# Kernel optimization log

Measured on AMD Instinct MI355X. Metric: run time of the kernel, lower is better.

## Reference

```python
import jax, jax.numpy as jnp
import numpy as np

B, D, C_IN = 2, 64, 4
N1, N2, N3, N4 = 32, 64, 96, 128
MQ, K = 1024, 5
DN = ('NCDHW', 'OIDHW', 'NCDHW')
PAD = [(2, 2)] * 3  # centered 5^3 kernel, matches Minkowski offsets in [-2, 2]


def setup_inputs() -> dict:
    rng = np.random.default_rng(0)
    mask = rng.random((B, D, D, D)) < 0.2
    x_feat = (rng.standard_normal((B, C_IN, D, D, D)) * mask[:, None]).astype(np.float32)
    Q_F = rng.random((B, MQ, 2)).astype(np.float32)  # per-point quality features (2 channels)

    def conv(cin, cout):
        w = (rng.standard_normal((cout, cin, K, K, K)) / np.sqrt(cin * K ** 3)).astype(np.float32)
        b = (0.01 * rng.standard_normal(cout)).astype(np.float32)
        return w, b

    def gdn(c):
        beta = np.ones(c, np.float32)
        gamma = (1e-4 * rng.random((c, c, K, K, K))).astype(np.float32)
        gamma[np.arange(c), np.arange(c), K // 2, K // 2, K // 2] += 0.1
        return beta, gamma

    w1, b1 = conv(C_IN, N1)
    w2, b2 = conv(N1, N2)
    w3, b3 = conv(N2, N3)
    w4, b4 = conv(N3, N4)
    beta1, gamma1 = gdn(N1)
    beta2, gamma2 = gdn(N2)
    beta3, gamma3 = gdn(N3)
    out = dict(x_feat=x_feat, mask=mask, Q_F=Q_F,
               w1=w1, b1=b1, w2=w2, b2=b2, w3=w3, b3=b3, w4=w4, b4=b4,
               beta1=beta1, gamma1=gamma1, beta2=beta2, gamma2=gamma2,
               beta3=beta3, gamma3=gamma3)
    return {k: jnp.asarray(v) for k, v in out.items()}


def _conv3d(x, w, b, stride):
    y = jax.lax.conv_general_dilated(x, w, (stride,) * 3, PAD, dimension_numbers=DN)
    return y + b[None, :, None, None, None]


def _pool_mask(m):
    # Minkowski stride-2 output coords = any occupied input in each 2x2x2 cell
    b, d = m.shape[0], m.shape[1]
    return m.reshape(b, d // 2, 2, d // 2, 2, d // 2, 2).max(axis=(2, 4, 6))


def _gdn(x, beta, gamma, scale, m):
    # conditional GDN: y = x / sqrt(beta + conv5(gamma, x^2)), scaled per batch by q[:,0]
    den = jax.lax.conv_general_dilated(x * x, gamma, (1, 1, 1), PAD, dimension_numbers=DN)
    y = x * jax.lax.rsqrt(beta[None, :, None, None, None] + den)
    return y * scale * m[:, None]


def reference(x_feat, mask, Q_F, w1, b1, w2, b2, w3, b3, w4, b4,
              beta1, gamma1, beta2, gamma2, beta3, gamma3):
    m0 = mask.astype(x_feat.dtype)
    q = jnp.mean(Q_F, axis=1)[None]                       # [1, B, 2]: per-batch mean of Q.F
    scale = q[0, :, 0][:, None, None, None, None]         # per-batch conditional scale

    c0 = m0.sum(axis=(1, 2, 3))                           # count_per_batch(x)
    m1 = _pool_mask(m0)
    x = _gdn(_conv3d(x_feat, w1, b1, 2) * m1[:, None], beta1, gamma1, scale, m1)
    c1 = m1.sum(axis=(1, 2, 3))
    m2 = _pool_mask(m1)
    x = _gdn(_conv3d(x, w2, b2, 2) * m2[:, None], beta2, gamma2, scale, m2)
    c2 = m2.sum(axis=(1, 2, 3))
    m3 = _pool_mask(m2)
    x = _gdn(_conv3d(x, w3, b3, 2) * m3[:, None], beta3, gamma3, scale, m3)
    x = _conv3d(x, w4, b4, 1) * m3[:, None]               # stride-1 conv keeps coords
    k = jnp.stack([c2, c1, c0]).astype(jnp.int32)         # k.reverse() in the original
    return x, q, k
```

## Files before the change

### kernel.cpp

```cpp
#include <hip/hip_runtime.h>
#include <math.h>

constexpr int Bn  = 2;
constexpr int CIN = 4;
constexpr int MQn = 1024;
constexpr int D0 = 64, D1 = 32, D2 = 16, D3 = 8;

constexpr int OUT_X = 0;
constexpr int OUT_Q = 131072;
constexpr int OUT_K = 131076;

constexpr size_t OFF_CNT   = 0;
constexpr size_t OFF_ZERO  = 8;
constexpr size_t OFF_D1    = 16;
constexpr size_t OFF_T2    = OFF_D1 + 2097152;
constexpr size_t OFF_D2    = OFF_T2 + 524288;
constexpr size_t OFF_T3    = OFF_D2 + 524288;
constexpr size_t OFF_D3    = OFF_T3 + 98304;
constexpr size_t ZERO_END  = OFF_D3 + 98304;
constexpr size_t OFF_SCALE = 3342360;
constexpr size_t OFF_M1    = 3342368;
constexpr size_t OFF_M2    = OFF_M1 + 65536;
constexpr size_t OFF_M3    = OFF_M2 + 8192;
constexpr size_t OFF_T1    = OFF_M3 + 1024;
constexpr size_t OFF_Y1    = OFF_T1 + 2097152;
constexpr size_t OFF_Y2    = OFF_Y1 + 2097152;
constexpr size_t OFF_SQ1   = OFF_Y2 + 524288;
constexpr size_t OFF_SQ2   = OFF_SQ1 + 1048576;
constexpr size_t OFF_SQ3   = OFF_SQ2 + 262144;
constexpr size_t OFF_Y3C   = OFF_SQ3 + 49152;
constexpr size_t OFF_W1T   = OFF_Y3C + 49152;
constexpr size_t OFF_W2T   = OFF_W1T + 16000;
constexpr size_t OFF_W3T   = OFF_W2T + 256000;
constexpr size_t OFF_WB1   = OFF_W3T + 768000;
constexpr size_t OFF_WB2   = OFF_WB1 + 64000;
constexpr size_t OFF_WB3   = OFF_WB2 + 256000;
constexpr size_t OFF_WB4   = OFF_WB3 + 576000;
constexpr size_t OFF_P2    = 12248736;
constexpr size_t OFF_Y1HL  = OFF_P2 + 3145728;
constexpr size_t OFF_WB2S  = OFF_Y1HL + 3145728;

typedef float v4f __attribute__((ext_vector_type(4)));
typedef __attribute__((ext_vector_type(8)))  short bf16x8v;
typedef __attribute__((ext_vector_type(16))) float f32x16v;

__device__ __forceinline__ void async_copy4(const float* g, float* l) {
    __builtin_amdgcn_global_load_lds(
        (const __attribute__((address_space(1))) void*)g,
        (__attribute__((address_space(3))) void*)l, 4, 0, 0);
}
__device__ __forceinline__ void async_copy16(const float* g, float* l) {
    __builtin_amdgcn_global_load_lds(
        (const __attribute__((address_space(1))) void*)g,
        (__attribute__((address_space(3))) void*)l, 16, 0, 0);
}
__device__ __forceinline__ unsigned short f2bf(float f) {
    unsigned u = __float_as_uint(f);
    return (unsigned short)((u + 0x7FFFu + ((u >> 16) & 1u)) >> 16);
}
__device__ __forceinline__ float bf2f(unsigned short h) {
    return __uint_as_float((unsigned)h << 16);
}

__global__ void qmean_kernel(const float* __restrict__ QF, float* __restrict__ out_q,
                             float* __restrict__ scale) {
    int b = blockIdx.x >> 1, c = blockIdx.x & 1;
    float s = 0.f;
    for (int m = threadIdx.x; m < MQn; m += blockDim.x)
        s += QF[(b * MQn + m) * 2 + c];
    __shared__ float sh[256];
    sh[threadIdx.x] = s;
    __syncthreads();
    for (int st = 128; st > 0; st >>= 1) {
        if (threadIdx.x < st) sh[threadIdx.x] += sh[threadIdx.x + st];
        __syncthreads();
    }
    if (threadIdx.x == 0) {
        float mean = sh[0] / (float)MQn;
        out_q[b * 2 + c] = mean;
        if (c == 0) scale[b] = mean;
    }
}

__global__ void mask_pool1_kernel(const float* __restrict__ xf, float* __restrict__ m1,
                                  float* __restrict__ c0) {
    int idx = blockIdx.x * blockDim.x + threadIdx.x;
    int b = idx >> 15;
    int v = idx & 32767;
    int oz = v >> 10, oy = (v >> 5) & 31, ox = v & 31;
    float cnt = 0.f, mx = 0.f;
    for (int dz = 0; dz < 2; ++dz)
        for (int dy = 0; dy < 2; ++dy)
            for (int dx = 0; dx < 2; ++dx) {
                int z = 2 * oz + dz, y = 2 * oy + dy, x = 2 * ox + dx;
                size_t base = (size_t)b * CIN * D0 * D0 * D0 + ((size_t)z * D0 + y) * D0 + x;
                bool occ = false;
                for (int c = 0; c < CIN; ++c)
                    occ = occ || (xf[base + (size_t)c * D0 * D0 * D0] != 0.f);
                if (occ) { cnt += 1.f; mx = 1.f; }
            }
    m1[idx] = mx;
    __shared__ float sh[256];
    sh[threadIdx.x] = cnt;
    __syncthreads();
    for (int st = 128; st > 0; st >>= 1) {
        if (threadIdx.x < st) sh[threadIdx.x] += sh[threadIdx.x + st];
        __syncthreads();
    }
    if (threadIdx.x == 0) atomicAdd(&c0[b], sh[0]);
}

__global__ void pool_kernel(const float* __restrict__ min_, float* __restrict__ mout,
                            float* __restrict__ cacc, int Din) {
    int Do = Din >> 1;
    int per = Do * Do * Do;
    int idx = blockIdx.x * blockDim.x + threadIdx.x;
    int b = idx / per;
    int v = idx % per;
    int oz = v / (Do * Do), oy = (v / Do) % Do, ox = v % Do;
    float s = 0.f, mx = 0.f;
    for (int dz = 0; dz < 2; ++dz)
        for (int dy = 0; dy < 2; ++dy)
            for (int dx = 0; dx < 2; ++dx) {
                float val = min_[(((size_t)b * Din + 2 * oz + dz) * Din + 2 * oy + dy) * Din + 2 * ox + dx];
                s += val;
                mx = fmaxf(mx, val);
            }
    mout[idx] = mx;
    __shared__ float sh[256];
    sh[threadIdx.x] = s;
    __syncthreads();
    for (int st = 128; st > 0; st >>= 1) {
        if (threadIdx.x < st) sh[threadIdx.x] += sh[threadIdx.x + st];
        __syncthreads();
    }
    if (threadIdx.x == 0) atomicAdd(&cacc[b], sh[0]);
}

__global__ void writek_kernel(const float* __restrict__ cnt, float* __restrict__ outk) {
    int i = threadIdx.x;
    if (i < 6) {
        int row = i >> 1, b = i & 1;
        float v = (row == 0) ? cnt[4 + b] : (row == 1 ? cnt[2 + b] : cnt[b]);
        outk[i] = v;
    }
}

constexpr int FS1 = 0,       FE1 = 16000;
constexpr int FS2 = 16000,   FE2 = 272000;
constexpr int FS3 = 272000,  FE3 = 1040000;
__global__ __launch_bounds__(256) void wtrans_all_kernel(
        const float* __restrict__ w1, const float* __restrict__ w2,
        const float* __restrict__ w3, float* __restrict__ ws) {
    int idx = blockIdx.x * 256 + threadIdx.x;
    if (idx >= FE3) return;
    const float* src; float* dst; int cin, local;
    if (idx < FE1)      { src = w1; dst = ws + OFF_W1T; cin = 4;  local = idx - FS1; }
    else if (idx < FE2) { src = w2; dst = ws + OFF_W2T; cin = 32; local = idx - FS2; }
    else                { src = w3; dst = ws + OFF_W3T; cin = 64; local = idx - FS3; }
    int per = cin * 125;
    int co = local / per;
    int r  = local % per;
    int ci = r / 125, tap = r % 125;
    int chunk = co >> 4, j = co & 15;
    dst[(((size_t)chunk * cin + ci) * 125 + tap) * 16 + j] = src[local];
}

constexpr int MS1 = 0,        ME1 = 128000;
constexpr int MS2 = 128000,   ME2 = 640000;
constexpr int MS3 = 640000,   ME3 = 1792000;
constexpr int MS4 = 1792000,  ME4 = 3328000;
__global__ __launch_bounds__(256) void mwtrans_all_kernel(
        const float* __restrict__ g1, const float* __restrict__ g2,
        const float* __restrict__ g3, const float* __restrict__ w4,
        float* __restrict__ ws) {
    int idx = blockIdx.x * 256 + threadIdx.x;
    if (idx >= ME4) return;
    const float* src; unsigned short* dst; int nchn, cin, o;
    if (idx < ME1)      { src = g1; dst = (unsigned short*)(ws + OFF_WB1); nchn = 1; cin = 32; o = idx - MS1; }
    else if (idx < ME2) { src = g2; dst = (unsigned short*)(ws + OFF_WB2); nchn = 2; cin = 64; o = idx - MS2; }
    else if (idx < ME3) { src = g3; dst = (unsigned short*)(ws + OFF_WB3); nchn = 3; cin = 96; o = idx - MS3; }
    else                { src = w4; dst = (unsigned short*)(ws + OFF_WB4); nchn = 4; cin = 96; o = idx - MS4; }
    int j  = o & 7;
    int kc = (o >> 3) & 1;
    int n  = (o >> 4) & 31;
    int q  = o >> 9;
    int tap = q % 125;
    int q2  = q / 125;
    int nch = q2 % nchn;
    int cs  = q2 / nchn;
    int co = nch * 32 + n;
    int ci = cs * 16 + kc * 8 + j;
    dst[o] = f2bf(src[((size_t)co * cin + ci) * 125 + tap]);
}

constexpr int W2S_N = 768000;
__global__ __launch_bounds__(256) void w2s_kernel(const float* __restrict__ w2,
        unsigned short* __restrict__ dst) {
    int o = blockIdx.x * 256 + threadIdx.x;
    if (o >= W2S_N) return;
    int j = o & 7; int kc = (o >> 3) & 1; int n = (o >> 4) & 31; int q = o >> 9;
    int tap = q % 125; int q2 = q / 125; int c = q2 & 1; int cs = q2 >> 1;
    int co = c * 32 + n;
    int e = cs * 16 + kc * 8 + j;
    int ci = e & 31;
    float wv = w2[((size_t)co * 32 + ci) * 125 + tap];
    unsigned short h = f2bf(wv);
    if (e >= 64) h = f2bf(wv - bf2f(h));
    dst[o] = h;
}

template<int CINt, int COUTt, int DIN, int DOUT, int STRIDE, int CIG, bool SQW>
__global__ __launch_bounds__(256, 4) void conv_tile_kernel(
    const float* __restrict__ in, const float* __restrict__ wt,
    const float* __restrict__ bb, const float* __restrict__ mask,
    const float* __restrict__ zerow, float* __restrict__ out,
    unsigned short* __restrict__ sqcl)
{
    constexpr int TZO = 4, TY = 8, TX = 8;
    constexpr int LZ = (STRIDE == 1) ? TZO + 4 : 2 * TZO + 3;
    constexpr int LY = (STRIDE == 1) ? TY + 4 : 2 * TY + 3;
    constexpr int LX = (STRIDE == 1) ? TX + 4 : 2 * TX + 3;
    constexpr int LXP = (STRIDE == 2) ? (LX + 1) / 2 : 0;
    constexpr int ROWLEN = (STRIDE == 2) ? 2 * LXP : LX;
    constexpr int LN = LZ * LY * ROWLEN;
    constexpr int NLOAD = (LN + 255) / 256;
    constexpr int PADN = NLOAD * 256;
    constexpr int NTZ = DOUT / TZO, NTY = DOUT / TY, NTX = DOUT / TX;
    constexpr int NT = NTZ * NTY * NTX;
    constexpr int NCHk = COUTt / 16;
    constexpr int CIPER = CINt / CIG;
    __shared__ float sh[2][PADN];
    __shared__ float wbuf[2][2048];

    int tile  = blockIdx.x % NT;
    int chunk = (blockIdx.x / NT) % NCHk;
    int cig   = (blockIdx.x / (NT * NCHk)) % CIG;
    int b     = blockIdx.x / (NT * NCHk * CIG);
    int tz0 = (tile / (NTY * NTX)) * TZO;
    int ty0 = ((tile / NTX) % NTY) * TY;
    int tx0 = (tile % NTX) * TX;
    int co0 = chunk * 16;

    int tid = threadIdx.x;
    int tx = tid & (TX - 1);
    int ty = (tid >> 3) & (TY - 1);
    int tz = tid >> 6;

    int iz0 = tz0 * STRIDE - 2, iy0 = ty0 * STRIDE - 2, ix0 = tx0 * STRIDE - 2;

    int goff[NLOAD];
#pragma unroll
    for (int k = 0; k < NLOAD; ++k) {
        int i = tid + k * 256;
        int c = i % ROWLEN; int rem = i / ROWLEN;
        int ly = rem % LY, lz = rem / LY;
        int lx;
        if (STRIDE == 2) { int p = c / LXP, xp = c % LXP; lx = 2 * xp + p; }
        else lx = c;
        int gz = iz0 + lz, gy = iy0 + ly, gx = ix0 + lx;
        bool valid = (i < LN) && (lx < LX) &&
                     (unsigned)gz < (unsigned)DIN && (unsigned)gy < (unsigned)DIN &&
                     (unsigned)gx < (unsigned)DIN;
        goff[k] = valid ? ((gz * DIN + gy) * DIN + gx) : -1;
    }

    int ci0 = cig * CIPER;
    auto stage = [&](int ci, int buf) {
        const float* base = in + (size_t)(b * CINt + ci) * DIN * DIN * DIN;
        float* dst = &sh[buf][0];
#pragma unroll
        for (int k = 0; k < NLOAD; ++k) {
            const float* g = (goff[k] >= 0) ? (base + goff[k]) : zerow;
            async_copy4(g, &dst[k * 256 + tid]);
        }
        const float* wsrc = wt + (size_t)(chunk * CINt + ci) * 2000;
#pragma unroll
        for (int k = 0; k < 2; ++k) {
            int f0 = (k * 256 + tid) * 4;
            const float* g = (f0 < 2000) ? (wsrc + f0) : zerow;
            async_copy16(g, &wbuf[buf][f0]);
        }
    };

    float acc[16];
#pragma unroll
    for (int j = 0; j < 16; ++j) acc[j] = 0.f;

    stage(ci0, 0);
#pragma unroll 1
    for (int i = 0; i < CIPER; ++i) {
        int cur = i & 1;
        __syncthreads();
        if (i + 1 < CIPER) stage(ci0 + i + 1, cur ^ 1);
        const float* shc = &sh[cur][0];
        const float* wb = &wbuf[cur][0];
#pragma unroll 1
        for (int kz = 0; kz < 5; ++kz) {
#pragma unroll 1
            for (int ky = 0; ky < 5; ++ky) {
                const float* rp = shc + ((tz * STRIDE + kz) * LY + ty * STRIDE + ky) * ROWLEN + tx;
                const float* wrow = wb + (kz * 5 + ky) * 5 * 16;
#pragma unroll
                for (int kx = 0; kx < 5; ++kx) {
                    float d = (STRIDE == 2) ? rp[(kx & 1) * LXP + (kx >> 1)] : rp[kx];
#pragma unroll
                    for (int q = 0; q < 4; ++q) {
                        v4f w = *(const v4f*)&wrow[kx * 16 + q * 4];
                        acc[4 * q + 0] = fmaf(d, w.x, acc[4 * q + 0]);
                        acc[4 * q + 1] = fmaf(d, w.y, acc[4 * q + 1]);
                        acc[4 * q + 2] = fmaf(d, w.z, acc[4 * q + 2]);
                        acc[4 * q + 3] = fmaf(d, w.w, acc[4 * q + 3]);
                    }
                }
            }
        }
    }

    int z = tz0 + tz, y = ty0 + ty, x = tx0 + tx;
    size_t sp = ((size_t)z * DOUT + y) * DOUT + x;
    if (CIG > 1) {
#pragma unroll
        for (int j = 0; j < 16; ++j) {
            size_t oidx = (size_t)(b * COUTt + co0 + j) * DOUT * DOUT * DOUT + sp;
            atomicAdd(&out[oidx], acc[j]);
        }
    } else {
        float mval = mask[(size_t)b * DOUT * DOUT * DOUT + sp];
        float vals[16];
#pragma unroll
        for (int j = 0; j < 16; ++j) {
            int co = co0 + j;
            size_t oidx = (size_t)(b * COUTt + co) * DOUT * DOUT * DOUT + sp;
            vals[j] = (acc[j] + bb[co]) * mval;
            out[oidx] = vals[j];
        }
        if (SQW) {
            bf16x8v s0, s1;
#pragma unroll
            for (int j = 0; j < 8; ++j) {
                s0[j] = (short)f2bf(vals[j] * vals[j]);
                s1[j] = (short)f2bf(vals[j + 8] * vals[j + 8]);
            }
            size_t cl = ((size_t)b * DOUT * DOUT * DOUT + sp) * COUTt + co0;
            *(bf16x8v*)(sqcl + cl) = s0;
            *(bf16x8v*)(sqcl + cl + 8) = s1;
        }
    }
}

__global__ __launch_bounds__(128) void gdn_cl1_kernel(const float* __restrict__ t,
        const float* __restrict__ den, const float* __restrict__ beta,
        const float* __restrict__ scale, unsigned short* __restrict__ yhl) {
    int idx = blockIdx.x * 128 + threadIdx.x;
    int sp = idx & 32767; int b = idx >> 15;
    float sc = scale[b];
    bf16x8v blk[12];
#pragma unroll
    for (int g = 0; g < 4; ++g) {
#pragma unroll
        for (int j = 0; j < 8; ++j) {
            int ci = g * 8 + j;
            size_t p = (size_t)(b * 32 + ci) * 32768 + sp;
            float v = t[p] * rsqrtf(beta[ci] + den[p]) * sc;
            unsigned short h = f2bf(v);
            blk[g][j] = (short)h;
            blk[4 + g][j] = (short)f2bf(v - bf2f(h));
            blk[8 + g][j] = (short)h;
        }
    }
    unsigned short* o = yhl + (size_t)idx * 96;
#pragma unroll
    for (int g = 0; g < 12; ++g) *(bf16x8v*)(o + g * 8) = blk[g];
}

template<int CINe, int COUTt, int DIN, int DOUT>
__global__ __launch_bounds__(256) void mconv_s2_kernel(
    const unsigned short* __restrict__ in,
    const unsigned short* __restrict__ wb,
    const float* __restrict__ zerow,
    float* __restrict__ pout)
{
    constexpr int NCH = COUTt / 32;
    constexpr int NTZ = DOUT / 4, NTY = DOUT / 4, NTX = DOUT / 8;
    constexpr int NT = NTZ * NTY * NTX * Bn;
    constexpr int VOX = DOUT * DOUT * DOUT;

    int tile = blockIdx.x % NT; int cs = blockIdx.x / NT;
    int r = tile;
    int tx0 = (r % NTX) * 8; r /= NTX;
    int ty0 = (r % NTY) * 4; r /= NTY;
    int tz0 = (r % NTZ) * 4; int b = r / NTZ;

    int tid = threadIdx.x;
    int lane = tid & 63, w = tid >> 6;
    int n = lane & 31, kc = lane >> 5;
    int oz = tz0 + w, oy = ty0 + (n >> 3), ox = tx0 + (n & 7);

    f32x16v acc[NCH];
#pragma unroll
    for (int c = 0; c < NCH; ++c)
#pragma unroll
        for (int i = 0; i < 16; ++i) acc[c][i] = 0.f;

#pragma unroll 1
    for (int kz = 0; kz < 5; ++kz) {
        int gz = 2 * oz + kz - 2;
        bool zok = (unsigned)gz < (unsigned)DIN;
#pragma unroll 1
        for (int ky = 0; ky < 5; ++ky) {
            int gy = 2 * oy + ky - 2;
            bool zyok = zok && ((unsigned)gy < (unsigned)DIN);
            long long rowbase = (((long long)(b * DIN + gz) * DIN + gy) * DIN) * CINe
                                + cs * 16 + kc * 8;
#pragma unroll
            for (int kx = 0; kx < 5; ++kx) {
                int gx = 2 * ox + kx - 2;
                bool ok = zyok && ((unsigned)gx < (unsigned)DIN);
                const unsigned short* g = ok ? in + (rowbase + (long long)gx * CINe)
                                             : (const unsigned short*)zerow;
                bf16x8v dfrag = *(const bf16x8v*)g;
                int tap = (kz * 5 + ky) * 5 + kx;
#pragma unroll
                for (int c = 0; c < NCH; ++c) {
                    const unsigned short* wp =
                        wb + (((size_t)(cs * NCH + c) * 125 + tap) << 9) + n * 16 + kc * 8;
                    bf16x8v wfrag = *(const bf16x8v*)wp;
                    acc[c] = __builtin_amdgcn_mfma_f32_32x32x16_bf16(wfrag, dfrag, acc[c], 0, 0, 0);
                }
            }
        }
    }

    int sp = (oz * DOUT + oy) * DOUT + ox;
#pragma unroll
    for (int c = 0; c < NCH; ++c) {
#pragma unroll
        for (int rr = 0; rr < 16; ++rr) {
            int co = c * 32 + (rr & 3) + 8 * (rr >> 2) + 4 * kc;
            pout[((size_t)(cs * Bn + b) * COUTt + co) * VOX + sp] = acc[c][rr];
        }
    }
}

__global__ __launch_bounds__(256) void red_epi2_kernel(const float* __restrict__ P,
        const float* __restrict__ bias, const float* __restrict__ mask,
        float* __restrict__ buf, unsigned short* __restrict__ sqcl) {
    constexpr int VOX = 4096;
    constexpr int NTOT = Bn * 64 * VOX;
    int idx = blockIdx.x * 256 + threadIdx.x;
    if (idx >= NTOT) return;
    int sp = idx % VOX;
    int co = (idx / VOX) & 63;
    int b = idx / (VOX * 64);
    float s = 0.f;
#pragma unroll
    for (int k = 0; k < 6; ++k) s += P[(size_t)k * NTOT + idx];
    float v = (s + bias[co]) * mask[b * VOX + sp];
    buf[idx] = v;
    sqcl[((size_t)b * VOX + sp) * 64 + co] = f2bf(v * v);
}

template<int CINt, int COUTt, int Dd, int TZ, int YB, int CIG, int ZSPL>
__global__ __launch_bounds__(256) void mconv_kernel(
    const unsigned short* __restrict__ in,
    const unsigned short* __restrict__ wb,
    const float* __restrict__ zerow,
    float* __restrict__ dout)
{
    constexpr int NCH = COUTt / 32;
    constexpr int LZ = TZ + 4, LYH = YB * 4 + 4, LXH = 12;
    constexpr int HV = LZ * LYH * LXH;
    constexpr int UN = 2 * HV;
    constexpr int NLOAD = (UN + 255) / 256;
    constexpr int NTZ = Dd / TZ, NTY = Dd / (YB * 4), NTX = Dd / 8;
    constexpr int NT = NTZ * NTY * NTX * Bn;
    __shared__ unsigned short lds[NLOAD * 256 * 8];

    int bid = blockIdx.x;
    int tile = bid % NT; int rest = bid / NT;
    int cs = rest % CIG; int zig = rest / CIG;
    int r = tile;
    int tx0 = (r % NTX) * 8; r /= NTX;
    int ty0 = (r % NTY) * (YB * 4); r /= NTY;
    int tz0 = (r % NTZ) * TZ; int b = r / NTZ;

    int tid = threadIdx.x;
    int iz0 = tz0 - 2, iy0 = ty0 - 2, ix0 = tx0 - 2;
#pragma unroll
    for (int k = 0; k < NLOAD; ++k) {
        int u = tid + k * 256;
        int v = u >> 1, half = u & 1;
        int lx = v % LXH; int t = v / LXH;
        int ly = t % LYH, lz = t / LYH;
        int gz = iz0 + lz, gy = iy0 + ly, gx = ix0 + lx;
        bool valid = (v < HV) &&
                     (unsigned)gz < (unsigned)Dd && (unsigned)gy < (unsigned)Dd &&
                     (unsigned)gx < (unsigned)Dd;
        const unsigned short* g = valid
            ? in + ((((size_t)b * Dd + gz) * Dd + gy) * Dd + gx) * CINt + cs * 16 + half * 8
            : (const unsigned short*)zerow;
        async_copy16((const float*)g, (float*)&lds[(size_t)u * 8]);
    }
    __syncthreads();

    int lane = tid & 63, w = tid >> 6;
    int zz = (YB == 1) ? w : (w >> 1);
    int yb = (YB == 1) ? 0 : (w & 1);
    int n = lane & 31, kc = lane >> 5;
    int vy = yb * 4 + (n >> 3), vx = n & 7;

    f32x16v acc[NCH];
#pragma unroll
    for (int c = 0; c < NCH; ++c)
#pragma unroll
        for (int i = 0; i < 16; ++i) acc[c][i] = 0.f;

    int kzlo = (ZSPL == 5) ? zig : 0;
    int kzhi = (ZSPL == 5) ? zig + 1 : 5;
#pragma unroll 1
    for (int kz = kzlo; kz < kzhi; ++kz) {
#pragma unroll 1
        for (int ky = 0; ky < 5; ++ky) {
            int hvrow = ((zz + kz) * LYH + (vy + ky)) * LXH + vx;
#pragma unroll
            for (int kx = 0; kx < 5; ++kx) {
                bf16x8v dfrag = *(const bf16x8v*)&lds[(size_t)(hvrow + kx) * 16 + kc * 8];
                int tap = (kz * 5 + ky) * 5 + kx;
#pragma unroll
                for (int c = 0; c < NCH; ++c) {
                    const unsigned short* wp =
                        wb + (((size_t)(cs * NCH + c) * 125 + tap) << 9) + n * 16 + kc * 8;
                    bf16x8v wfrag = *(const bf16x8v*)wp;
                    acc[c] = __builtin_amdgcn_mfma_f32_32x32x16_bf16(wfrag, dfrag, acc[c], 0, 0, 0);
                }
            }
        }
    }

    int sp = ((tz0 + zz) * Dd + (ty0 + vy)) * Dd + (tx0 + vx);
#pragma unroll
    for (int c = 0; c < NCH; ++c) {
#pragma unroll
        for (int rr = 0; rr < 16; ++rr) {
            int co = c * 32 + (rr & 3) + 8 * (rr >> 2) + 4 * kc;
            atomicAdd(&dout[(size_t)(b * COUTt + co) * Dd * Dd * Dd + sp], acc[c][rr]);
        }
    }
}

template<int COUTt, int DOUT, bool SQ>
__global__ __launch_bounds__(256) void conv_epi_kernel(float* __restrict__ buf,
        const float* __restrict__ bias, const float* __restrict__ mask,
        unsigned short* __restrict__ sqcl) {
    constexpr int VOX = DOUT * DOUT * DOUT;
    int idx = blockIdx.x * 256 + threadIdx.x;
    if (idx >= Bn * COUTt * VOX) return;
    int sp = idx % VOX;
    int co = (idx / VOX) % COUTt;
    int b = idx / (VOX * COUTt);
    float v = (buf[idx] + bias[co]) * mask[b * VOX + sp];
    buf[idx] = v;
    if (SQ) sqcl[((size_t)b * VOX + sp) * COUTt + co] = f2bf(v * v);
}

template<int COUTt, int DOUT, bool CL>
__global__ __launch_bounds__(256) void gdn_epi_kernel(const float* __restrict__ t,
        const float* __restrict__ den, const float* __restrict__ beta,
        const float* __restrict__ scale, float* __restrict__ y,
        unsigned short* __restrict__ ycl) {
    constexpr int VOX = DOUT * DOUT * DOUT;
    int idx = blockIdx.x * 256 + threadIdx.x;
    if (idx >= Bn * COUTt * VOX) return;
    int sp = idx % VOX;
    int co = (idx / VOX) % COUTt;
    int b = idx / (VOX * COUTt);
    float v = t[idx] * rsqrtf(beta[co] + den[idx]) * scale[b];
    if (CL) ycl[((size_t)b * VOX + sp) * COUTt + co] = f2bf(v);
    else    y[idx] = v;
}

extern "C" void kernel_launch(void* const* d_in, const int* in_sizes, int n_in,
                              void* d_out, int out_size, void* d_ws, size_t ws_size,
                              hipStream_t stream) {
    const float* x_feat = (const float*)d_in[0];
    const float* QF     = (const float*)d_in[2];
    const float* w1 = (const float*)d_in[3];  const float* b1 = (const float*)d_in[4];
    const float* w2 = (const float*)d_in[5];  const float* b2 = (const float*)d_in[6];
    const float* w3 = (const float*)d_in[7];  const float* b3 = (const float*)d_in[8];
    const float* w4 = (const float*)d_in[9];  const float* b4 = (const float*)d_in[10];
    const float* beta1 = (const float*)d_in[11]; const float* gamma1 = (const float*)d_in[12];
    const float* beta2 = (const float*)d_in[13]; const float* gamma2 = (const float*)d_in[14];
    const float* beta3 = (const float*)d_in[15]; const float* gamma3 = (const float*)d_in[16];

    float* out = (float*)d_out;
    float* ws = (float*)d_ws;
    float* cnt   = ws + OFF_CNT;
    float* zerow = ws + OFF_ZERO;
    float* scale = ws + OFF_SCALE;
    float* m1 = ws + OFF_M1;  float* m2 = ws + OFF_M2;  float* m3 = ws + OFF_M3;
    float* t1 = ws + OFF_T1;  float* d1 = ws + OFF_D1;
    float* t2 = ws + OFF_T2;  float* d2 = ws + OFF_D2;  float* y2 = ws + OFF_Y2;
    float* t3 = ws + OFF_T3;  float* d3 = ws + OFF_D3;
    float* p2 = ws + OFF_P2;
    unsigned short* sq1 = (unsigned short*)(ws + OFF_SQ1);
    unsigned short* sq2 = (unsigned short*)(ws + OFF_SQ2);
    unsigned short* sq3 = (unsigned short*)(ws + OFF_SQ3);
    unsigned short* y3c = (unsigned short*)(ws + OFF_Y3C);
    unsigned short* y1hl = (unsigned short*)(ws + OFF_Y1HL);
    float* w1T = ws + OFF_W1T; float* w3T = ws + OFF_W3T;
    unsigned short* wb1 = (unsigned short*)(ws + OFF_WB1);
    unsigned short* wb2 = (unsigned short*)(ws + OFF_WB2);
    unsigned short* wb3 = (unsigned short*)(ws + OFF_WB3);
    unsigned short* wb4 = (unsigned short*)(ws + OFF_WB4);
    unsigned short* wb2s = (unsigned short*)(ws + OFF_WB2S);

    hipMemsetAsync(ws, 0, ZERO_END * sizeof(float), stream);
    hipMemsetAsync(out + OUT_X, 0, 131072 * sizeof(float), stream);

    qmean_kernel<<<4, 256, 0, stream>>>(QF, out + OUT_Q, scale);
    mask_pool1_kernel<<<256, 256, 0, stream>>>(x_feat, m1, cnt + 0);
    pool_kernel<<<32, 256, 0, stream>>>(m1, m2, cnt + 2, D1);
    pool_kernel<<<4, 256, 0, stream>>>(m2, m3, cnt + 4, D2);
    writek_kernel<<<1, 64, 0, stream>>>(cnt, out + OUT_K);

    wtrans_all_kernel<<<(FE3 + 255) / 256, 256, 0, stream>>>(w1, w2, w3, ws);
    mwtrans_all_kernel<<<(ME4 + 255) / 256, 256, 0, stream>>>(gamma1, gamma2, gamma3, w4, ws);
    w2s_kernel<<<(W2S_N + 255) / 256, 256, 0, stream>>>(w2, wb2s);

    conv_tile_kernel<4, 32, 64, 32, 2, 1, true>
        <<<512, 256, 0, stream>>>(x_feat, w1T, b1, m1, zerow, t1, sq1);
    mconv_kernel<32, 32, 32, 4, 1, 2, 1>
        <<<1024, 256, 0, stream>>>(sq1, wb1, zerow, d1);
    gdn_cl1_kernel<<<512, 128, 0, stream>>>(t1, d1, beta1, scale, y1hl);

    mconv_s2_kernel<96, 64, 32, 16>
        <<<64 * 6, 256, 0, stream>>>(y1hl, wb2s, zerow, p2);
    red_epi2_kernel<<<2048, 256, 0, stream>>>(p2, b2, m2, t2, sq2);
    mconv_kernel<64, 64, 16, 4, 1, 4, 1>
        <<<256, 256, 0, stream>>>(sq2, wb2, zerow, d2);
    gdn_epi_kernel<64, 16, false><<<2048, 256, 0, stream>>>(t2, d2, beta2, scale, y2, nullptr);

    conv_tile_kernel<64, 96, 16, 8, 2, 8, false>
        <<<192, 256, 0, stream>>>(y2, w3T, nullptr, nullptr, zerow, t3, nullptr);
    conv_epi_kernel<96, 8, true><<<384, 256, 0, stream>>>(t3, b3, m3, sq3);
    mconv_kernel<96, 96, 8, 2, 2, 6, 5>
        <<<240, 256, 0, stream>>>(sq3, wb3, zerow, d3);
    gdn_epi_kernel<96, 8, true><<<384, 256, 0, stream>>>(t3, d3, beta3, scale, nullptr, y3c);

    mconv_kernel<96, 128, 8, 2, 2, 6, 5>
        <<<240, 256, 0, stream>>>(y3c, wb4, zerow, out + OUT_X);
    conv_epi_kernel<128, 8, false><<<512, 256, 0, stream>>>(out + OUT_X, b4, m3, nullptr);
}
```

Measured before the change: 472.2 us.

## Move first stride-2 conv to bf16 MFMA with split hi/lo channels-last input

Replaces the fp32 tiled first convolution with an MFMA kernel. The input is first converted to channels-last bf16 hi/lo pairs packed into 8 K-lanes, and the weights get a matching hi/lo layout, so each tap is a single 32x32x16 MFMA. The epilogue applies bias and mask and writes both t1 and the bf16 squared features. This adds two preprocessing kernels and reads global memory directly without LDS reuse, and the bf16 split trades a little precision (the lo*lo term is dropped) for matrix-core throughput.

```diff
diff --git a/kernel.cpp b/kernel.cpp
--- a/kernel.cpp
+++ b/kernel.cpp
@@ -39,9 +39,11 @@
 constexpr size_t OFF_P2    = 12248736;
 constexpr size_t OFF_Y1HL  = OFF_P2 + 3145728;
 constexpr size_t OFF_WB2S  = OFF_Y1HL + 3145728;
+constexpr size_t OFF_WB1S  = OFF_WB2S + 384000;
 
 typedef float v4f __attribute__((ext_vector_type(4)));
 typedef __attribute__((ext_vector_type(8)))  short bf16x8v;
+typedef __attribute__((ext_vector_type(4)))  short bf16x4v;
 typedef __attribute__((ext_vector_type(16))) float f32x16v;
 
 __device__ __forceinline__ void async_copy4(const float* g, float* l) {
@@ -210,6 +212,101 @@
     dst[o] = h;
 }
 
+constexpr int W1S_N = 64000;
+__global__ __launch_bounds__(256) void w1s_kernel(const float* __restrict__ w1,
+        unsigned short* __restrict__ dst) {
+    int o = blockIdx.x * 256 + threadIdx.x;
+    if (o >= W1S_N) return;
+    int j = o & 7; int kc = (o >> 3) & 1; int n = (o >> 4) & 31; int tap = o >> 9;
+    int ci = j & 3;
+    unsigned short h;
+    float wv = w1[((size_t)n * 4 + ci) * 125 + tap];
+    unsigned short hi = f2bf(wv);
+    if (kc == 0)       h = hi;
+    else if (j < 4)    h = f2bf(wv - bf2f(hi));
+    else               h = 0;
+    dst[o] = h;
+}
+
+__global__ __launch_bounds__(256) void xcl_kernel(const float* __restrict__ xf,
+        unsigned short* __restrict__ xcl) {
+    int idx = blockIdx.x * 256 + threadIdx.x;
+    int s = idx & 262143; int b = idx >> 18;
+    bf16x8v o;
+#pragma unroll
+    for (int ci = 0; ci < 4; ++ci) {
+        float f = xf[((size_t)(b * 4 + ci) << 18) + s];
+        unsigned short h = f2bf(f);
+        o[ci] = (short)h;
+        o[4 + ci] = (short)f2bf(f - bf2f(h));
+    }
+    *(bf16x8v*)(xcl + (size_t)idx * 8) = o;
+}
+
+__global__ __launch_bounds__(256) void mconv1_s2_kernel(
+    const unsigned short* __restrict__ xcl,
+    const unsigned short* __restrict__ wb,
+    const float* __restrict__ bias, const float* __restrict__ mask,
+    const float* __restrict__ zerow,
+    float* __restrict__ t1, unsigned short* __restrict__ sqcl)
+{
+    constexpr int DIN = 64, DOUT = 32;
+    constexpr int NTX = 4, NTY = 8;
+    int r = blockIdx.x;
+    int tx0 = (r % NTX) * 8; r /= NTX;
+    int ty0 = (r % NTY) * 4; r /= NTY;
+    int tz0 = (r % 8) * 4;   int b = r / 8;
+
+    int tid = threadIdx.x;
+    int lane = tid & 63, w = tid >> 6;
+    int n = lane & 31, kc = lane >> 5;
+    int oz = tz0 + w, oy = ty0 + (n >> 3), ox = tx0 + (n & 7);
+
+    f32x16v acc;
+#pragma unroll
+    for (int i = 0; i < 16; ++i) acc[i] = 0.f;
+
+#pragma unroll 1
+    for (int kz = 0; kz < 5; ++kz) {
+        int gz = 2 * oz + kz - 2;
+        bool zok = (unsigned)gz < (unsigned)DIN;
+#pragma unroll 1
+        for (int ky = 0; ky < 5; ++ky) {
+            int gy = 2 * oy + ky - 2;
+            bool zyok = zok && ((unsigned)gy < (unsigned)DIN);
+            long long rowbase = (((long long)(b * DIN + gz) * DIN + gy) * DIN) * 8;
+#pragma unroll
+            for (int kx = 0; kx < 5; ++kx) {
+                int gx = 2 * ox + kx - 2;
+                bool ok = zyok && ((unsigned)gx < (unsigned)DIN);
+                const unsigned short* g = ok ? xcl + (rowbase + (long long)gx * 8)
+                                             : (const unsigned short*)zerow;
+                bf16x8v dfrag = *(const bf16x8v*)g;
+                int tap = (kz * 5 + ky) * 5 + kx;
+                const unsigned short* wp = wb + ((size_t)tap << 9) + n * 16 + kc * 8;
+                bf16x8v wfrag = *(const bf16x8v*)wp;
+                acc = __builtin_amdgcn_mfma_f32_32x32x16_bf16(wfrag, dfrag, acc, 0, 0, 0);
+            }
+        }
+    }
+
+    int sp = (oz * DOUT + oy) * DOUT + ox;
+    float mval = mask[b * DOUT * DOUT * DOUT + sp];
+#pragma unroll
+    for (int q = 0; q < 4; ++q) {
+        int co0 = 8 * q + 4 * kc;
+        bf16x4v s4;
+#pragma unroll
+        for (int j = 0; j < 4; ++j) {
+            int co = co0 + j;
+            float v = (acc[4 * q + j] + bias[co]) * mval;
+            t1[(size_t)(b * 32 + co) * 32768 + sp] = v;
+            s4[j] = (short)f2bf(v * v);
+        }
+        *(bf16x4v*)(sqcl + ((size_t)(b * 32768 + sp)) * 32 + co0) = s4;
+    }
+}
+
 template<int CINt, int COUTt, int DIN, int DOUT, int STRIDE, int CIG, bool SQW>
 __global__ __launch_bounds__(256, 4) void conv_tile_kernel(
     const float* __restrict__ in, const float* __restrict__ wt,
@@ -608,12 +705,14 @@
     unsigned short* sq3 = (unsigned short*)(ws + OFF_SQ3);
     unsigned short* y3c = (unsigned short*)(ws + OFF_Y3C);
     unsigned short* y1hl = (unsigned short*)(ws + OFF_Y1HL);
-    float* w1T = ws + OFF_W1T; float* w3T = ws + OFF_W3T;
+    unsigned short* xcl = (unsigned short*)(ws + OFF_Y1);
+    float* w3T = ws + OFF_W3T;
     unsigned short* wb1 = (unsigned short*)(ws + OFF_WB1);
     unsigned short* wb2 = (unsigned short*)(ws + OFF_WB2);
     unsigned short* wb3 = (unsigned short*)(ws + OFF_WB3);
     unsigned short* wb4 = (unsigned short*)(ws + OFF_WB4);
     unsigned short* wb2s = (unsigned short*)(ws + OFF_WB2S);
+    unsigned short* wb1s = (unsigned short*)(ws + OFF_WB1S);
 
     hipMemsetAsync(ws, 0, ZERO_END * sizeof(float), stream);
     hipMemsetAsync(out + OUT_X, 0, 131072 * sizeof(float), stream);
@@ -627,9 +726,10 @@
     wtrans_all_kernel<<<(FE3 + 255) / 256, 256, 0, stream>>>(w1, w2, w3, ws);
     mwtrans_all_kernel<<<(ME4 + 255) / 256, 256, 0, stream>>>(gamma1, gamma2, gamma3, w4, ws);
     w2s_kernel<<<(W2S_N + 255) / 256, 256, 0, stream>>>(w2, wb2s);
-
-    conv_tile_kernel<4, 32, 64, 32, 2, 1, true>
-        <<<512, 256, 0, stream>>>(x_feat, w1T, b1, m1, zerow, t1, sq1);
+    w1s_kernel<<<(W1S_N + 255) / 256, 256, 0, stream>>>(w1, wb1s);
+    xcl_kernel<<<2048, 256, 0, stream>>>(x_feat, xcl);
+
+    mconv1_s2_kernel<<<512, 256, 0, stream>>>(xcl, wb1s, b1, m1, zerow, t1, sq1);
     mconv_kernel<32, 32, 32, 4, 1, 2, 1>
         <<<1024, 256, 0, stream>>>(sq1, wb1, zerow, d1);
     gdn_cl1_kernel<<<512, 128, 0, stream>>>(t1, d1, beta1, scale, y1hl);
```

After: 468.4 us. No clear change (-0.8%).
